# Kernel optimization log

Measured on AMD Instinct MI355X. Metric: run time of the kernel, lower is better.

The kernel has to match this reference:

```python
import jax, jax.numpy as jnp
import numpy as np

D_MODEL = 1024
D_HEAD = 64
M_BITS = 32


def setup_inputs() -> dict:
    key = jax.random.key(0)
    ks = jax.random.split(key, 6)
    B, N, M = 2, 2048, 2048
    Q = jax.random.normal(ks[0], (B, N, D_MODEL), dtype=jnp.float32)
    K = jax.random.normal(ks[1], (B, M, D_MODEL), dtype=jnp.float32)
    V = jax.random.normal(ks[2], (B, M, D_MODEL), dtype=jnp.float32)
    s = 1.0 / np.sqrt(D_MODEL)
    Wq = jax.random.normal(ks[3], (D_MODEL, M_BITS), dtype=jnp.float32) * s
    Wk = jax.random.normal(ks[4], (D_MODEL, M_BITS), dtype=jnp.float32) * s
    Wv = jax.random.normal(ks[5], (D_MODEL, D_HEAD), dtype=jnp.float32) * s
    temperature = jnp.ones((1,), dtype=jnp.float32)
    return {"Q": Q, "K": K, "V": V, "Wq": Wq, "Wk": Wk, "Wv": Wv,
            "temperature": temperature}


def tropical_matmul(A, Bt):
    # A: [B, N, m], Bt: [B, M, m] (already transposed form of [B, m, M])
    # (A \odot B)_{ij} = min_k (A_ik + B_kj)
    return jnp.min(A[:, :, None, :] + Bt[:, None, :, :], axis=-1)  # [B, N, M]


def reference(Q, K, V, Wq, Wk, Wv, temperature):
    # REWA tropical encoders (continuous): linear projections to m_bits
    Qt = jnp.einsum('bnd,dm->bnm', Q, Wq)   # [B, N, m_bits]
    Kt = jnp.einsum('bsd,dm->bsm', K, Wk)   # [B, M, m_bits]
    Vp = jnp.einsum('bsd,dh->bsh', V, Wv)   # [B, M, d_head]
    # tropical (min-plus) scores, negated so shorter paths score higher
    scores = -tropical_matmul(Qt, Kt)       # [B, N, M]
    scores = scores / jax.nn.softplus(temperature[0])
    attn = jax.nn.softmax(scores, axis=-1)  # [B, N, M]
    out = jnp.einsum('bnm,bmh->bnh', attn, Vp)  # [B, N, d_head]
    return out, attn
```

## Files before the change

### kernel.cpp

```cpp
#include <hip/hip_runtime.h>
#include <math.h>

#define DM 1024
#define NB 2048
#define MBITS 32
#define DH 64

typedef __attribute__((ext_vector_type(4))) float floatx4;
typedef __attribute__((ext_vector_type(8))) short shortx8;

__device__ __forceinline__ unsigned short f32_to_bf16(float f) {
    union { float f; unsigned u; } v; v.f = f;
    unsigned r = v.u + 0x7FFF + ((v.u >> 16) & 1);
    return (unsigned short)(r >> 16);
}

__device__ __forceinline__ void split2(float x0, float x1, unsigned& hp, unsigned& lp) {
    union { float f; unsigned u; } a, b; a.f = x0; b.f = x1;
    unsigned h0 = a.u & 0xFFFF0000u, h1 = b.u & 0xFFFF0000u;
    union { unsigned u; float f; } hf0, hf1; hf0.u = h0; hf1.u = h1;
    union { float f; unsigned u; } c, d;
    c.f = x0 - hf0.f;
    d.f = x1 - hf1.f;
    hp = (h0 >> 16) | h1;
    lp = (c.u >> 16) | (d.u & 0xFFFF0000u);
}

__global__ __launch_bounds__(256) void wprep_kernel(
    const float* __restrict__ Wq, const float* __restrict__ Wk,
    const float* __restrict__ Wv, unsigned short* __restrict__ Wf)
{
    int wv = blockIdx.x * 4 + (threadIdx.x >> 6);
    int l  = threadIdx.x & 63;
    const float* W; int C, kc32, ct;
    if (wv < 64)       { W = Wq; C = 32; kc32 = wv >> 1;  ct = wv & 1; }
    else if (wv < 128) { W = Wk; C = 32; int z = wv - 64;  kc32 = z >> 1; ct = z & 1; }
    else               { W = Wv; C = 64; int z = wv - 128; kc32 = z >> 2; ct = z & 3; }
    int k0 = kc32 * 32 + (l >> 4) * 8;
    int c  = ct * 16 + (l & 15);
    float x[8];
    #pragma unroll
    for (int j = 0; j < 8; ++j) x[j] = W[(size_t)(k0 + j) * C + c];
    unsigned hp[4], lp[4];
    #pragma unroll
    for (int j2 = 0; j2 < 4; ++j2) split2(x[2 * j2], x[2 * j2 + 1], hp[j2], lp[j2]);
    uint4 hv; hv.x = hp[0]; hv.y = hp[1]; hv.z = hp[2]; hv.w = hp[3];
    uint4 lv; lv.x = lp[0]; lv.y = lp[1]; lv.z = lp[2]; lv.w = lp[3];
    *(uint4*)&Wf[(size_t)wv * 1024 + l * 8]       = hv;
    *(uint4*)&Wf[(size_t)wv * 1024 + 512 + l * 8] = lv;
}

__global__ __launch_bounds__(512) void proj_mfma2_kernel(
    const float* __restrict__ Q, const float* __restrict__ K, const float* __restrict__ V,
    const unsigned short* __restrict__ Wf,
    float* __restrict__ Qt, float* __restrict__ KtT, unsigned short* __restrict__ VpT)
{
    __shared__ float red[8][64][16];

    int gb = blockIdx.x;
    int job = gb >> 8, tile = gb & 255;
    int r0 = tile * 16;
    const float* X = (job == 0) ? Q : (job == 1) ? K : V;
    int ntct  = (job == 2) ? 4 : 2;
    int pbase = job << 6;
    int t = threadIdx.x, w = t >> 6, l = t & 63;
    int lrow = l & 15, lq = l >> 4;

    const float* xrow = &X[(size_t)(r0 + lrow) * DM + w * 128 + lq * 8];

    floatx4 acc[4];
    #pragma unroll
    for (int i = 0; i < 4; ++i) acc[i] = (floatx4){0.f, 0.f, 0.f, 0.f};

    #pragma unroll
    for (int s = 0; s < 4; ++s) {
        floatx4 g0 = *(const floatx4*)(xrow + s * 32);
        floatx4 g1 = *(const floatx4*)(xrow + s * 32 + 4);
        union { unsigned u[4]; shortx8 v; } ahi, alo;
        split2(g0.x, g0.y, ahi.u[0], alo.u[0]);
        split2(g0.z, g0.w, ahi.u[1], alo.u[1]);
        split2(g1.x, g1.y, ahi.u[2], alo.u[2]);
        split2(g1.z, g1.w, ahi.u[3], alo.u[3]);
        int kc32 = w * 4 + s;
        #pragma unroll
        for (int ct = 0; ct < 4; ++ct) {
            if (ct >= ntct) break;
            int p = pbase + kc32 * ntct + ct;
            const unsigned short* wp = &Wf[(size_t)p * 1024 + l * 8];
            shortx8 bhi = *(const shortx8*)wp;
            shortx8 blo = *(const shortx8*)(wp + 512);
            acc[ct] = __builtin_amdgcn_mfma_f32_16x16x32_bf16(ahi.v, bhi, acc[ct], 0, 0, 0);
            acc[ct] = __builtin_amdgcn_mfma_f32_16x16x32_bf16(ahi.v, blo, acc[ct], 0, 0, 0);
            acc[ct] = __builtin_amdgcn_mfma_f32_16x16x32_bf16(alo.v, bhi, acc[ct], 0, 0, 0);
        }
    }

    #pragma unroll
    for (int ct = 0; ct < 4; ++ct) {
        if (ct >= ntct) break;
        #pragma unroll
        for (int r = 0; r < 4; ++r) red[w][l][ct * 4 + r] = acc[ct][r];
    }
    __syncthreads();

    int r = w & 3, ct0 = w >> 2;
    int row = r0 + lq * 4 + r;
    if (job == 0) {
        float v = red[0][l][ct0 * 4 + r] + red[1][l][ct0 * 4 + r]
                + red[2][l][ct0 * 4 + r] + red[3][l][ct0 * 4 + r]
                + red[4][l][ct0 * 4 + r] + red[5][l][ct0 * 4 + r]
                + red[6][l][ct0 * 4 + r] + red[7][l][ct0 * 4 + r];
        Qt[(size_t)row * MBITS + ct0 * 16 + lrow] = v;
    } else if (job == 1) {
        int bb = row >> 11, j = row & 2047;
        float v = red[0][l][ct0 * 4 + r] + red[1][l][ct0 * 4 + r]
                + red[2][l][ct0 * 4 + r] + red[3][l][ct0 * 4 + r]
                + red[4][l][ct0 * 4 + r] + red[5][l][ct0 * 4 + r]
                + red[6][l][ct0 * 4 + r] + red[7][l][ct0 * 4 + r];
        KtT[(size_t)bb * (MBITS * NB) + (size_t)(ct0 * 16 + lrow) * NB + j] = v;
    } else {
        int bb = row >> 11, j = row & 2047;
        #pragma unroll
        for (int cti = 0; cti < 2; ++cti) {
            int ct = ct0 + 2 * cti;
            float v = red[0][l][ct * 4 + r] + red[1][l][ct * 4 + r]
                    + red[2][l][ct * 4 + r] + red[3][l][ct * 4 + r]
                    + red[4][l][ct * 4 + r] + red[5][l][ct * 4 + r]
                    + red[6][l][ct * 4 + r] + red[7][l][ct * 4 + r];
            VpT[(size_t)bb * (DH * NB) + (size_t)(ct * 16 + lrow) * NB + j] = f32_to_bf16(v);
        }
    }
}

__global__ __attribute__((amdgpu_waves_per_eu(4, 4))) __launch_bounds__(1024)
void fused_score_out_kernel(
    const float* __restrict__ Qt, const float* __restrict__ KtT,
    const unsigned short* __restrict__ VpT, const float* __restrict__ temp,
    float* __restrict__ outp, float* __restrict__ attn)
{
    __shared__ unsigned short Elds[16][2056];
    __shared__ float redsum[16][8];

    const int b  = blockIdx.y;
    const int i0 = blockIdx.x * 16;
    const int t  = threadIdx.x;
    const int w  = t >> 6, l = t & 63;

    const float tv = temp[0];
    const float c2 = -(1.0f / log1pf(__expf(tv))) * 1.44269504088896340736f;

    {
        const int rg = w & 1;
        const int jc = w >> 1;
        const int j0 = jc * 256 + l * 4;

        const float* Qb = &Qt[(size_t)(b * NB + i0 + rg * 8) * MBITS];
        const float* Kb = &KtT[(size_t)b * (MBITS * NB) + j0];

        float m[8][4];
        #pragma unroll
        for (int r = 0; r < 8; ++r)
            #pragma unroll
            for (int jj = 0; jj < 4; ++jj) m[r][jj] = 1e30f;

        floatx4 kA[4], kB[4];
        #pragma unroll
        for (int k2 = 0; k2 < 4; ++k2)
            kA[k2] = *(const floatx4*)(Kb + (size_t)k2 * NB);

        #pragma unroll 1
        for (int kc = 0; kc < 4; ++kc) {
            #pragma unroll
            for (int k2 = 0; k2 < 4; ++k2)
                kB[k2] = *(const floatx4*)(Kb + (size_t)(kc * 8 + 4 + k2) * NB);
            #pragma unroll
            for (int r = 0; r < 8; ++r) {
                floatx4 q = *(const floatx4*)(Qb + r * MBITS + kc * 8);
                #pragma unroll
                for (int k2 = 0; k2 < 4; ++k2) {
                    float qq = q[k2];
                    m[r][0] = fminf(m[r][0], qq + kA[k2].x);
                    m[r][1] = fminf(m[r][1], qq + kA[k2].y);
                    m[r][2] = fminf(m[r][2], qq + kA[k2].z);
                    m[r][3] = fminf(m[r][3], qq + kA[k2].w);
                }
            }
            if (kc < 3) {
                #pragma unroll
                for (int k2 = 0; k2 < 4; ++k2)
                    kA[k2] = *(const floatx4*)(Kb + (size_t)(kc * 8 + 8 + k2) * NB);
            }
            #pragma unroll
            for (int r = 0; r < 8; ++r) {
                floatx4 q = *(const floatx4*)(Qb + r * MBITS + kc * 8 + 4);
                #pragma unroll
                for (int k2 = 0; k2 < 4; ++k2) {
                    float qq = q[k2];
                    m[r][0] = fminf(m[r][0], qq + kB[k2].x);
                    m[r][1] = fminf(m[r][1], qq + kB[k2].y);
                    m[r][2] = fminf(m[r][2], qq + kB[k2].z);
                    m[r][3] = fminf(m[r][3], qq + kB[k2].w);
                }
            }
        }

        #pragma unroll
        for (int r = 0; r < 8; ++r) {
            float e0 = exp2f(c2 * m[r][0]);
            float e1 = exp2f(c2 * m[r][1]);
            float e2 = exp2f(c2 * m[r][2]);
            float e3 = exp2f(c2 * m[r][3]);
            uint2 pk;
            pk.x = (unsigned)f32_to_bf16(e0) | ((unsigned)f32_to_bf16(e1) << 16);
            pk.y = (unsigned)f32_to_bf16(e2) | ((unsigned)f32_to_bf16(e3) << 16);
            *(uint2*)&Elds[rg * 8 + r][j0] = pk;
            float s = (e0 + e1) + (e2 + e3);
            #pragma unroll
            for (int off = 1; off < 64; off <<= 1) s += __shfl_xor(s, off, 64);
            if (l == 0) redsum[w][r] = s;
        }
    }
    __syncthreads();

    const int mrow = l & 15, q4 = l >> 4;
    const int hh  = (w & 3) * 16 + mrow;
    const int kg  = w >> 2;
    floatx4 acc = {0.f, 0.f, 0.f, 0.f};
    const unsigned short* Vb = &VpT[(size_t)b * (DH * NB) + (size_t)hh * NB];

    #pragma unroll
    for (int jc2 = 0; jc2 < 8; ++jc2) {
        #pragma unroll
        for (int t2 = 0; t2 < 2; ++t2) {
            int ks = kg * 2 + t2;
            int joff = jc2 * 256 + ks * 32 + q4 * 8;
            shortx8 a  = *(const shortx8*)&Elds[mrow][joff];
            shortx8 bf = *(const shortx8*)&Vb[joff];
            acc = __builtin_amdgcn_mfma_f32_16x16x32_bf16(a, bf, acc, 0, 0, 0);
        }
    }

    {
        float s = 0.f;
        #pragma unroll
        for (int g = 0; g < 8; ++g) s += redsum[(w >> 3) + 2 * g][w & 7];
        float iv = 1.0f / s;
        #pragma unroll
        for (int u = 0; u < 8; ++u) {
            int j = u * 256 + l * 4;
            uint2 pk = *(const uint2*)&Elds[w][j];
            union { unsigned u; float f; } x0, x1, x2, x3;
            x0.u = pk.x << 16; x1.u = pk.x & 0xFFFF0000u;
            x2.u = pk.y << 16; x3.u = pk.y & 0xFFFF0000u;
            floatx4 o;
            o.x = x0.f * iv; o.y = x1.f * iv; o.z = x2.f * iv; o.w = x3.f * iv;
            *(floatx4*)&attn[(size_t)(b * NB + i0 + w) * 2048 + j] = o;
        }
    }
    __syncthreads();

    float* redCf = (float*)&Elds[0][0];
    if (w >= 4) *(floatx4*)&redCf[(((w - 4) * 64) + l) * 4] = acc;
    __syncthreads();
    if (w < 4) {
        floatx4 v0 = *(const floatx4*)&redCf[((w * 64) + l) * 4];
        floatx4 v1 = *(const floatx4*)&redCf[(((w + 4) * 64) + l) * 4];
        floatx4 v2 = *(const floatx4*)&redCf[(((w + 8) * 64) + l) * 4];
        #pragma unroll
        for (int r = 0; r < 4; ++r) {
            int irow = q4 * 4 + r;
            float sr = 0.f;
            #pragma unroll
            for (int g = 0; g < 8; ++g) sr += redsum[(irow >> 3) + 2 * g][irow & 7];
            float ivr = 1.0f / sr;
            float v = ((acc[r] + v0[r]) + (v1[r] + v2[r]));
            outp[(size_t)(b * NB + i0 + irow) * DH + w * 16 + mrow] = v * ivr;
        }
    }
}

extern "C" void kernel_launch(void* const* d_in, const int* in_sizes, int n_in,
                              void* d_out, int out_size, void* d_ws, size_t ws_size,
                              hipStream_t stream) {
    (void)in_sizes; (void)n_in; (void)out_size; (void)ws_size;
    const float* Q    = (const float*)d_in[0];
    const float* K    = (const float*)d_in[1];
    const float* V    = (const float*)d_in[2];
    const float* Wq   = (const float*)d_in[3];
    const float* Wk   = (const float*)d_in[4];
    const float* Wv   = (const float*)d_in[5];
    const float* temp = (const float*)d_in[6];

    float* outp = (float*)d_out;
    float* attn = outp + 2 * 2048 * 64;

    char* ws = (char*)d_ws;
    float*          Qt  = (float*)(ws);
    float*          KtT = (float*)(ws + 524288);
    unsigned short* Wf  = (unsigned short*)(ws + 1179648);
    unsigned short* VpT = (unsigned short*)(ws + 1703936);

    wprep_kernel<<<64, 256, 0, stream>>>(Wq, Wk, Wv, Wf);
    proj_mfma2_kernel<<<768, 512, 0, stream>>>(Q, K, V, Wf, Qt, KtT, VpT);
    fused_score_out_kernel<<<dim3(128, 2), 1024, 0, stream>>>(Qt, KtT, VpT, temp, outp, attn);
}
```

Measured before the change: 143.8 us.

## Merge weight prep, projections and attention into one cooperative kernel

Replaces the three-kernel sequence with a single cooperative launch of 256 blocks of 1024 threads, using grid-wide syncs between weight splitting, the Q/K/V projections and the fused score/softmax/output stage. Each block now projects 16 rows of Q, K and V itself, with the same LDS reused for the reduction buffers and the score tile. This is meant to remove kernel launch gaps and tail effects between stages. In exchange it pays grid barrier costs, has only 256 blocks doing the projection work that previously used 768, and requires all blocks to be co-resident.

```diff
diff --git a/kernel.cpp b/kernel.cpp
--- a/kernel.cpp
+++ b/kernel.cpp
@@ -1,5 +1,8 @@
 #include <hip/hip_runtime.h>
+#include <hip/hip_cooperative_groups.h>
 #include <math.h>
+
+namespace cg = cooperative_groups;
 
 #define DM 1024
 #define NB 2048
@@ -26,125 +29,155 @@
     lp = (c.u >> 16) | (d.u & 0xFFFF0000u);
 }
 
-__global__ __launch_bounds__(256) void wprep_kernel(
-    const float* __restrict__ Wq, const float* __restrict__ Wk,
-    const float* __restrict__ Wv, unsigned short* __restrict__ Wf)
+__global__ __attribute__((amdgpu_waves_per_eu(4, 4))) __launch_bounds__(1024)
+void mono_kernel(
+    const float* __restrict__ Q, const float* __restrict__ K, const float* __restrict__ V,
+    const float* __restrict__ Wq, const float* __restrict__ Wk, const float* __restrict__ Wv,
+    const float* __restrict__ temp, unsigned short* __restrict__ Wf,
+    float* __restrict__ Qt, float* __restrict__ KtT, unsigned short* __restrict__ VpT,
+    float* __restrict__ outp, float* __restrict__ attn)
 {
-    int wv = blockIdx.x * 4 + (threadIdx.x >> 6);
-    int l  = threadIdx.x & 63;
-    const float* W; int C, kc32, ct;
-    if (wv < 64)       { W = Wq; C = 32; kc32 = wv >> 1;  ct = wv & 1; }
-    else if (wv < 128) { W = Wk; C = 32; int z = wv - 64;  kc32 = z >> 1; ct = z & 1; }
-    else               { W = Wv; C = 64; int z = wv - 128; kc32 = z >> 2; ct = z & 3; }
-    int k0 = kc32 * 32 + (l >> 4) * 8;
-    int c  = ct * 16 + (l & 15);
-    float x[8];
-    #pragma unroll
-    for (int j = 0; j < 8; ++j) x[j] = W[(size_t)(k0 + j) * C + c];
-    unsigned hp[4], lp[4];
-    #pragma unroll
-    for (int j2 = 0; j2 < 4; ++j2) split2(x[2 * j2], x[2 * j2 + 1], hp[j2], lp[j2]);
-    uint4 hv; hv.x = hp[0]; hv.y = hp[1]; hv.z = hp[2]; hv.w = hp[3];
-    uint4 lv; lv.x = lp[0]; lv.y = lp[1]; lv.z = lp[2]; lv.w = lp[3];
-    *(uint4*)&Wf[(size_t)wv * 1024 + l * 8]       = hv;
-    *(uint4*)&Wf[(size_t)wv * 1024 + 512 + l * 8] = lv;
-}
-
-__global__ __launch_bounds__(512) void proj_mfma2_kernel(
-    const float* __restrict__ Q, const float* __restrict__ K, const float* __restrict__ V,
-    const unsigned short* __restrict__ Wf,
-    float* __restrict__ Qt, float* __restrict__ KtT, unsigned short* __restrict__ VpT)
-{
-    __shared__ float red[8][64][16];
-
-    int gb = blockIdx.x;
-    int job = gb >> 8, tile = gb & 255;
-    int r0 = tile * 16;
-    const float* X = (job == 0) ? Q : (job == 1) ? K : V;
-    int ntct  = (job == 2) ? 4 : 2;
-    int pbase = job << 6;
-    int t = threadIdx.x, w = t >> 6, l = t & 63;
-    int lrow = l & 15, lq = l >> 4;
-
-    const float* xrow = &X[(size_t)(r0 + lrow) * DM + w * 128 + lq * 8];
-
-    floatx4 acc[4];
-    #pragma unroll
-    for (int i = 0; i < 4; ++i) acc[i] = (floatx4){0.f, 0.f, 0.f, 0.f};
-
-    #pragma unroll
-    for (int s = 0; s < 4; ++s) {
-        floatx4 g0 = *(const floatx4*)(xrow + s * 32);
-        floatx4 g1 = *(const floatx4*)(xrow + s * 32 + 4);
-        union { unsigned u[4]; shortx8 v; } ahi, alo;
-        split2(g0.x, g0.y, ahi.u[0], alo.u[0]);
-        split2(g0.z, g0.w, ahi.u[1], alo.u[1]);
-        split2(g1.x, g1.y, ahi.u[2], alo.u[2]);
-        split2(g1.z, g1.w, ahi.u[3], alo.u[3]);
-        int kc32 = w * 4 + s;
-        #pragma unroll
-        for (int ct = 0; ct < 4; ++ct) {
-            if (ct >= ntct) break;
-            int p = pbase + kc32 * ntct + ct;
-            const unsigned short* wp = &Wf[(size_t)p * 1024 + l * 8];
-            shortx8 bhi = *(const shortx8*)wp;
-            shortx8 blo = *(const shortx8*)(wp + 512);
-            acc[ct] = __builtin_amdgcn_mfma_f32_16x16x32_bf16(ahi.v, bhi, acc[ct], 0, 0, 0);
-            acc[ct] = __builtin_amdgcn_mfma_f32_16x16x32_bf16(ahi.v, blo, acc[ct], 0, 0, 0);
-            acc[ct] = __builtin_amdgcn_mfma_f32_16x16x32_bf16(alo.v, bhi, acc[ct], 0, 0, 0);
-        }
-    }
-
-    #pragma unroll
-    for (int ct = 0; ct < 4; ++ct) {
-        if (ct >= ntct) break;
-        #pragma unroll
-        for (int r = 0; r < 4; ++r) red[w][l][ct * 4 + r] = acc[ct][r];
-    }
-    __syncthreads();
-
-    int r = w & 3, ct0 = w >> 2;
-    int row = r0 + lq * 4 + r;
-    if (job == 0) {
-        float v = red[0][l][ct0 * 4 + r] + red[1][l][ct0 * 4 + r]
-                + red[2][l][ct0 * 4 + r] + red[3][l][ct0 * 4 + r]
-                + red[4][l][ct0 * 4 + r] + red[5][l][ct0 * 4 + r]
-                + red[6][l][ct0 * 4 + r] + red[7][l][ct0 * 4 + r];
-        Qt[(size_t)row * MBITS + ct0 * 16 + lrow] = v;
-    } else if (job == 1) {
-        int bb = row >> 11, j = row & 2047;
-        float v = red[0][l][ct0 * 4 + r] + red[1][l][ct0 * 4 + r]
-                + red[2][l][ct0 * 4 + r] + red[3][l][ct0 * 4 + r]
-                + red[4][l][ct0 * 4 + r] + red[5][l][ct0 * 4 + r]
-                + red[6][l][ct0 * 4 + r] + red[7][l][ct0 * 4 + r];
-        KtT[(size_t)bb * (MBITS * NB) + (size_t)(ct0 * 16 + lrow) * NB + j] = v;
-    } else {
+    __shared__ __align__(16) char smem[65792];
+    __shared__ float redsum[16][8];
+
+    float (*red)[64][16]       = (float (*)[64][16])smem;
+    unsigned short (*Elds)[2056] = (unsigned short (*)[2056])smem;
+
+    cg::grid_group grid = cg::this_grid();
+
+    const int bi = blockIdx.x;
+    const int t  = threadIdx.x;
+    const int w  = t >> 6, l = t & 63;
+    const int lrow = l & 15, lq = l >> 4;
+
+    if (bi < 64 && w < 4) {
+        int wv = bi * 4 + w;
+        const float* W; int C, kc32, ct;
+        if (wv < 64)       { W = Wq; C = 32; kc32 = wv >> 1;  ct = wv & 1; }
+        else if (wv < 128) { W = Wk; C = 32; int z = wv - 64;  kc32 = z >> 1; ct = z & 1; }
+        else               { W = Wv; C = 64; int z = wv - 128; kc32 = z >> 2; ct = z & 3; }
+        int k0 = kc32 * 32 + lq * 8;
+        int c  = ct * 16 + lrow;
+        float x[8];
+        #pragma unroll
+        for (int j = 0; j < 8; ++j) x[j] = W[(size_t)(k0 + j) * C + c];
+        unsigned hp[4], lp[4];
+        #pragma unroll
+        for (int j2 = 0; j2 < 4; ++j2) split2(x[2 * j2], x[2 * j2 + 1], hp[j2], lp[j2]);
+        uint4 hv; hv.x = hp[0]; hv.y = hp[1]; hv.z = hp[2]; hv.w = hp[3];
+        uint4 lv; lv.x = lp[0]; lv.y = lp[1]; lv.z = lp[2]; lv.w = lp[3];
+        *(uint4*)&Wf[(size_t)wv * 1024 + l * 8]       = hv;
+        *(uint4*)&Wf[(size_t)wv * 1024 + 512 + l * 8] = lv;
+    }
+    grid.sync();
+
+    const int r0 = bi * 16;
+    {
+        const int job = w >> 3;
+        const int jw  = w & 7;
+        const float* X = job ? K : Q;
+        const int pbase = job << 6;
+
+        const float* xrow = &X[(size_t)(r0 + lrow) * DM + jw * 128 + lq * 8];
+
+        floatx4 acc[2];
+        acc[0] = (floatx4){0.f, 0.f, 0.f, 0.f};
+        acc[1] = (floatx4){0.f, 0.f, 0.f, 0.f};
+
+        #pragma unroll
+        for (int s = 0; s < 4; ++s) {
+            floatx4 g0 = *(const floatx4*)(xrow + s * 32);
+            floatx4 g1 = *(const floatx4*)(xrow + s * 32 + 4);
+            union { unsigned u[4]; shortx8 v; } ahi, alo;
+            split2(g0.x, g0.y, ahi.u[0], alo.u[0]);
+            split2(g0.z, g0.w, ahi.u[1], alo.u[1]);
+            split2(g1.x, g1.y, ahi.u[2], alo.u[2]);
+            split2(g1.z, g1.w, ahi.u[3], alo.u[3]);
+            int kc32 = jw * 4 + s;
+            #pragma unroll
+            for (int ct = 0; ct < 2; ++ct) {
+                int p = pbase + kc32 * 2 + ct;
+                const unsigned short* wp = &Wf[(size_t)p * 1024 + l * 8];
+                shortx8 bhi = *(const shortx8*)wp;
+                shortx8 blo = *(const shortx8*)(wp + 512);
+                acc[ct] = __builtin_amdgcn_mfma_f32_16x16x32_bf16(ahi.v, bhi, acc[ct], 0, 0, 0);
+                acc[ct] = __builtin_amdgcn_mfma_f32_16x16x32_bf16(ahi.v, blo, acc[ct], 0, 0, 0);
+                acc[ct] = __builtin_amdgcn_mfma_f32_16x16x32_bf16(alo.v, bhi, acc[ct], 0, 0, 0);
+            }
+        }
+        #pragma unroll
+        for (int ct = 0; ct < 2; ++ct)
+            #pragma unroll
+            for (int r = 0; r < 4; ++r) red[w][l][ct * 4 + r] = acc[ct][r];
+    }
+    __syncthreads();
+    {
+        const int job = w >> 3, jw = w & 7;
+        const int rr = jw & 3, ct0 = jw >> 2;
+        const int base = job * 8;
+        int row = r0 + lq * 4 + rr;
+        float v = 0.f;
+        #pragma unroll
+        for (int u = 0; u < 8; ++u) v += red[base + u][l][ct0 * 4 + rr];
+        if (job == 0) {
+            Qt[(size_t)row * MBITS + ct0 * 16 + lrow] = v;
+        } else {
+            int bb = row >> 11, j = row & 2047;
+            KtT[(size_t)bb * (MBITS * NB) + (size_t)(ct0 * 16 + lrow) * NB + j] = v;
+        }
+    }
+    __syncthreads();
+
+    if (w < 8) {
+        const float* xrow = &V[(size_t)(r0 + lrow) * DM + w * 128 + lq * 8];
+        floatx4 acc[4];
+        #pragma unroll
+        for (int i = 0; i < 4; ++i) acc[i] = (floatx4){0.f, 0.f, 0.f, 0.f};
+
+        #pragma unroll
+        for (int s = 0; s < 4; ++s) {
+            floatx4 g0 = *(const floatx4*)(xrow + s * 32);
+            floatx4 g1 = *(const floatx4*)(xrow + s * 32 + 4);
+            union { unsigned u[4]; shortx8 v; } ahi, alo;
+            split2(g0.x, g0.y, ahi.u[0], alo.u[0]);
+            split2(g0.z, g0.w, ahi.u[1], alo.u[1]);
+            split2(g1.x, g1.y, ahi.u[2], alo.u[2]);
+            split2(g1.z, g1.w, ahi.u[3], alo.u[3]);
+            int kc32 = w * 4 + s;
+            #pragma unroll
+            for (int ct = 0; ct < 4; ++ct) {
+                int p = 128 + kc32 * 4 + ct;
+                const unsigned short* wp = &Wf[(size_t)p * 1024 + l * 8];
+                shortx8 bhi = *(const shortx8*)wp;
+                shortx8 blo = *(const shortx8*)(wp + 512);
+                acc[ct] = __builtin_amdgcn_mfma_f32_16x16x32_bf16(ahi.v, bhi, acc[ct], 0, 0, 0);
+                acc[ct] = __builtin_amdgcn_mfma_f32_16x16x32_bf16(ahi.v, blo, acc[ct], 0, 0, 0);
+                acc[ct] = __builtin_amdgcn_mfma_f32_16x16x32_bf16(alo.v, bhi, acc[ct], 0, 0, 0);
+            }
+        }
+        #pragma unroll
+        for (int ct = 0; ct < 4; ++ct)
+            #pragma unroll
+            for (int r = 0; r < 4; ++r) red[w][l][ct * 4 + r] = acc[ct][r];
+    }
+    __syncthreads();
+    if (w < 8) {
+        int r = w & 3, ct0 = w >> 2;
+        int row = r0 + lq * 4 + r;
         int bb = row >> 11, j = row & 2047;
         #pragma unroll
         for (int cti = 0; cti < 2; ++cti) {
             int ct = ct0 + 2 * cti;
-            float v = red[0][l][ct * 4 + r] + red[1][l][ct * 4 + r]
-                    + red[2][l][ct * 4 + r] + red[3][l][ct * 4 + r]
-                    + red[4][l][ct * 4 + r] + red[5][l][ct * 4 + r]
-                    + red[6][l][ct * 4 + r] + red[7][l][ct * 4 + r];
+            float v = 0.f;
+            #pragma unroll
+            for (int u = 0; u < 8; ++u) v += red[u][l][ct * 4 + r];
             VpT[(size_t)bb * (DH * NB) + (size_t)(ct * 16 + lrow) * NB + j] = f32_to_bf16(v);
         }
     }
-}
-
-__global__ __attribute__((amdgpu_waves_per_eu(4, 4))) __launch_bounds__(1024)
-void fused_score_out_kernel(
-    const float* __restrict__ Qt, const float* __restrict__ KtT,
-    const unsigned short* __restrict__ VpT, const float* __restrict__ temp,
-    float* __restrict__ outp, float* __restrict__ attn)
-{
-    __shared__ unsigned short Elds[16][2056];
-    __shared__ float redsum[16][8];
-
-    const int b  = blockIdx.y;
-    const int i0 = blockIdx.x * 16;
-    const int t  = threadIdx.x;
-    const int w  = t >> 6, l = t & 63;
+    grid.sync();
+
+    const int b  = bi >> 7;
+    const int i0 = (bi & 127) * 16;
 
     const float tv = temp[0];
     const float c2 = -(1.0f / log1pf(__expf(tv))) * 1.44269504088896340736f;
@@ -225,7 +258,7 @@
     const int mrow = l & 15, q4 = l >> 4;
     const int hh  = (w & 3) * 16 + mrow;
     const int kg  = w >> 2;
-    floatx4 acc = {0.f, 0.f, 0.f, 0.f};
+    floatx4 acc2 = {0.f, 0.f, 0.f, 0.f};
     const unsigned short* Vb = &VpT[(size_t)b * (DH * NB) + (size_t)hh * NB];
 
     #pragma unroll
@@ -236,7 +269,7 @@
             int joff = jc2 * 256 + ks * 32 + q4 * 8;
             shortx8 a  = *(const shortx8*)&Elds[mrow][joff];
             shortx8 bf = *(const shortx8*)&Vb[joff];
-            acc = __builtin_amdgcn_mfma_f32_16x16x32_bf16(a, bf, acc, 0, 0, 0);
+            acc2 = __builtin_amdgcn_mfma_f32_16x16x32_bf16(a, bf, acc2, 0, 0, 0);
         }
     }
 
@@ -260,7 +293,7 @@
     __syncthreads();
 
     float* redCf = (float*)&Elds[0][0];
-    if (w >= 4) *(floatx4*)&redCf[(((w - 4) * 64) + l) * 4] = acc;
+    if (w >= 4) *(floatx4*)&redCf[(((w - 4) * 64) + l) * 4] = acc2;
     __syncthreads();
     if (w < 4) {
         floatx4 v0 = *(const floatx4*)&redCf[((w * 64) + l) * 4];
@@ -273,7 +306,7 @@
             #pragma unroll
             for (int g = 0; g < 8; ++g) sr += redsum[(irow >> 3) + 2 * g][irow & 7];
             float ivr = 1.0f / sr;
-            float v = ((acc[r] + v0[r]) + (v1[r] + v2[r]));
+            float v = ((acc2[r] + v0[r]) + (v1[r] + v2[r]));
             outp[(size_t)(b * NB + i0 + irow) * DH + w * 16 + mrow] = v * ivr;
         }
     }
@@ -300,7 +333,11 @@
     unsigned short* Wf  = (unsigned short*)(ws + 1179648);
     unsigned short* VpT = (unsigned short*)(ws + 1703936);
 
-    wprep_kernel<<<64, 256, 0, stream>>>(Wq, Wk, Wv, Wf);
-    proj_mfma2_kernel<<<768, 512, 0, stream>>>(Q, K, V, Wf, Qt, KtT, VpT);
-    fused_score_out_kernel<<<dim3(128, 2), 1024, 0, stream>>>(Qt, KtT, VpT, temp, outp, attn);
+    void* kargs[] = {
+        (void*)&Q, (void*)&K, (void*)&V, (void*)&Wq, (void*)&Wk, (void*)&Wv,
+        (void*)&temp, (void*)&Wf, (void*)&Qt, (void*)&KtT, (void*)&VpT,
+        (void*)&outp, (void*)&attn
+    };
+    hipLaunchCooperativeKernel((const void*)mono_kernel, dim3(256), dim3(1024),
+                               kargs, 0, stream);
 }
```

Result: slower. 225.4 us (+56.8%).
